# Kernel optimization log

Hardware: AMD Instinct MI355X
Metric: run time of the kernel (lower is better)

The kernel has to match this reference:

```python
import jax, jax.numpy as jnp
import numpy as np

VOCAB = 100000
TAGS = 48
EMB = 256
HID = 512
B, S = 64, 512


def setup_inputs() -> dict:
    key = jax.random.key(0)
    ks = jax.random.split(key, 7)
    sc_e = 1.0 / np.sqrt(EMB)
    sc_h = 1.0 / np.sqrt(HID)
    return {
        "x": jax.random.randint(ks[0], (B, S), 0, VOCAB),
        "emb": jax.random.normal(ks[1], (VOCAB, EMB), jnp.float32),
        "W_ih": jax.random.uniform(ks[2], (4 * HID, EMB), jnp.float32, -sc_e, sc_e),
        "W_hh": jax.random.uniform(ks[3], (4 * HID, HID), jnp.float32, -sc_h, sc_h),
        "b_hh": jax.random.uniform(ks[4], (4 * HID,), jnp.float32, -sc_h, sc_h),
        "fc_W": jax.random.uniform(ks[5], (TAGS, HID), jnp.float32, -sc_h, sc_h),
        "fc_b": jax.random.uniform(ks[6], (TAGS,), jnp.float32, -sc_h, sc_h),
    }


def reference(x, emb, W_ih, W_hh, b_hh, fc_W, fc_b):
    # Embedding lookup: [B,S] -> [B,S,E]
    xe = emb[x]
    # Precompute input projection for all timesteps: [B,S,4H]
    px = jnp.einsum("bse,ge->bsg", xe, W_ih)
    H = W_hh.shape[1]
    Bc = x.shape[0]
    h0 = jnp.zeros((Bc, H), px.dtype)
    c0 = jnp.zeros((Bc, H), px.dtype)

    def step(carry, pxt):
        h, c = carry
        # recurrent dropout prob = 0 -> mask is identity
        gates = pxt + h @ W_hh.T + b_hh  # [B,4H]
        i, f, g, o = jnp.split(gates, 4, axis=-1)
        i = jax.nn.sigmoid(i)
        f = jax.nn.sigmoid(f)
        g = jnp.tanh(g)
        o = jax.nn.sigmoid(o)
        c = f * c + i * g
        h = o * jnp.tanh(c)
        return (h, c), h

    _, hs = jax.lax.scan(step, (h0, c0), jnp.swapaxes(px, 0, 1))
    hs = jnp.swapaxes(hs, 0, 1)  # [B,S,H]
    logits = hs @ fc_W.T + fc_b  # [B,S,TAGS]
    return jax.nn.log_softmax(logits, axis=2)
```

## Files before the change

### kernel.cpp

```cpp
#include <hip/hip_runtime.h>
#include <hip/hip_bf16.h>
#include <hip/hip_fp16.h>

typedef __attribute__((ext_vector_type(8))) short short8;
typedef __attribute__((ext_vector_type(4))) float f32x4;
typedef __attribute__((ext_vector_type(2))) unsigned long long ull2;

#define Hh 512
#define Bb 64
#define Ss 512
#define Gg 2048
#define NROW 32768

static __device__ inline short f2bf(float f) {
    union { float f; unsigned u; } v; v.f = f;
    unsigned r = (v.u + 0x7FFFu + ((v.u >> 16) & 1u)) >> 16;
    return (short)r;
}

static __device__ inline short8 pack_bf8(const float* p) {
    f32x4 u0 = *(const f32x4*)p;
    f32x4 u1 = *(const f32x4*)(p + 4);
    short8 t;
    t[0] = f2bf(u0[0]); t[1] = f2bf(u0[1]); t[2] = f2bf(u0[2]); t[3] = f2bf(u0[3]);
    t[4] = f2bf(u1[0]); t[5] = f2bf(u1[1]); t[6] = f2bf(u1[2]); t[7] = f2bf(u1[3]);
    return t;
}

static __device__ inline float fsigmoid(float x) {
    return __builtin_amdgcn_rcpf(1.f + __builtin_amdgcn_exp2f(x * -1.44269504088896f));
}
static __device__ inline float ftanh(float x) {
    float xc = fminf(fmaxf(x, -15.f), 15.f);
    float e = __builtin_amdgcn_exp2f(xc * 2.88539008177793f);
    return (e - 1.f) / (e + 1.f);
}

__global__ __launch_bounds__(256)
void prep_bf16(const float* __restrict__ wih, const float* __restrict__ fcw,
               short* __restrict__ wih_bf, short* __restrict__ fcw_bf) {
    const int n1 = Gg * 256;
    const int n2 = 48 * Hh;
    for (int i = blockIdx.x * blockDim.x + threadIdx.x; i < n1 + n2;
         i += gridDim.x * blockDim.x) {
        if (i < n1) wih_bf[i] = f2bf(wih[i]);
        else        fcw_bf[i - n1] = f2bf(fcw[i - n1]);
    }
}

__global__ __launch_bounds__(256)
void px_kernel(const int* __restrict__ x, const float* __restrict__ emb,
               const short* __restrict__ wih_bf, const float* __restrict__ bhh,
               _Float16* __restrict__ px) {
    const int w = threadIdx.x >> 6, lane = threadIdx.x & 63;
    const int lr = lane & 15, lc = lane >> 4;
    const int r0 = blockIdx.x * 64 + w * 16;

    short8 a[8];
    const int tok = x[r0 + lr];
    const float* arow = emb + (long)tok * 256;
#pragma unroll
    for (int ks = 0; ks < 8; ks++)
        a[ks] = pack_bf8(arow + ks * 32 + lc * 8);

    for (int g0 = 0; g0 < Gg; g0 += 16) {
        f32x4 acc = {0.f, 0.f, 0.f, 0.f};
#pragma unroll
        for (int ks = 0; ks < 8; ks++) {
            short8 b = *(const short8*)(wih_bf + (g0 + lr) * 256 + ks * 32 + lc * 8);
            acc = __builtin_amdgcn_mfma_f32_16x16x32_bf16(a[ks], b, acc, 0, 0, 0);
        }
        const float bias = bhh[g0 + lr];
#pragma unroll
        for (int i = 0; i < 4; i++) {
            const int r = r0 + lc * 4 + i;
            const int bb = r >> 9, s = r & 511;
            px[((long)s * Bb + bb) * Gg + g0 + lr] = (_Float16)(acc[i] + bias);
        }
    }
}

__global__ __launch_bounds__(512)
void lstm_kernel(const float* __restrict__ whh, const _Float16* __restrict__ px,
                 unsigned int* __restrict__ hbuf32,
                 unsigned int* __restrict__ hs32,
                 int* __restrict__ flags) {
    const int cl  = blockIdx.x & 3;
    const int wgc = blockIdx.x >> 2;
    const int b0 = cl * 16;
    const int J0 = wgc * 64;
    const int w = threadIdx.x >> 6;
    const int lane = threadIdx.x & 63;
    const int lr = lane & 15, lc = lane >> 4;
    const int gt = w & 3;
    const int Jsub = (w >> 2) * 32;

    __shared__ float gates[4][16][64];
    __shared__ __align__(16) unsigned int hlds[16 * 256];

    short8 wf[2][16];
#pragma unroll
    for (int u = 0; u < 2; u++)
#pragma unroll
        for (int ks = 0; ks < 16; ks++)
            wf[u][ks] = pack_bf8(whh + (long)(gt * Hh + J0 + Jsub + u * 16 + lr) * Hh + ks * 32 + lc * 8);

    const int eb = threadIdx.x >> 5;
    const int jp = threadIdx.x & 31;
    float c0 = 0.f, c1 = 0.f;

    const int gr0 = gt * Hh + J0 + Jsub + lr;
    float pf[2][4];
#pragma unroll
    for (int u = 0; u < 2; u++)
#pragma unroll
        for (int i = 0; i < 4; i++)
            pf[u][i] = (float)px[((long)0 * Bb + b0 + lc * 4 + i) * Gg + gr0 + u * 16];

    int* const myflag = flags + cl * 32 + wgc;

#pragma unroll 1
    for (int t = 0; t < Ss; t++) {
        if (threadIdx.x < 8) {
            const int* fp = flags + cl * 32 + threadIdx.x;
            while (__hip_atomic_load(fp, __ATOMIC_RELAXED, __HIP_MEMORY_SCOPE_AGENT) < t)
                __builtin_amdgcn_s_sleep(1);
        }
        __syncthreads();

        {
            const unsigned long long* hb =
                (const unsigned long long*)hbuf32 + (long)(t & 1) * (Bb * Hh / 4);
            int m = threadIdx.x;
#pragma unroll
            for (int k = 0; k < 2; k++, m += 512) {
                const int row = m >> 6;
                const int c   = (m & 63) * 4;
                const unsigned long long* p = hb + (long)(b0 + row) * 128 + (c >> 1);
                unsigned long long q0 = __hip_atomic_load(p,     __ATOMIC_RELAXED, __HIP_MEMORY_SCOPE_AGENT);
                unsigned long long q1 = __hip_atomic_load(p + 1, __ATOMIC_RELAXED, __HIP_MEMORY_SCOPE_AGENT);
                const int sw = c ^ ((row & 7) << 2);
                ull2 q; q[0] = q0; q[1] = q1;
                *(ull2*)&hlds[row * 256 + sw] = q;
            }
        }
        __syncthreads();

        f32x4 acc[2];
#pragma unroll
        for (int u = 0; u < 2; u++) {
            acc[u][0] = pf[u][0]; acc[u][1] = pf[u][1];
            acc[u][2] = pf[u][2]; acc[u][3] = pf[u][3];
        }

#pragma unroll
        for (int ks = 0; ks < 16; ks++) {
            const int c = ks * 16 + lc * 4;
            const short8 af = *(const short8*)&hlds[lr * 256 + (c ^ ((lr & 7) << 2))];
            acc[0] = __builtin_amdgcn_mfma_f32_16x16x32_bf16(af, wf[0][ks], acc[0], 0, 0, 0);
            acc[1] = __builtin_amdgcn_mfma_f32_16x16x32_bf16(af, wf[1][ks], acc[1], 0, 0, 0);
        }

#pragma unroll
        for (int u = 0; u < 2; u++)
#pragma unroll
            for (int i = 0; i < 4; i++)
                gates[gt][lc * 4 + i][Jsub + u * 16 + lr] = acc[u][i];
        __syncthreads();

        unsigned hpack;
        {
            const int j = jp * 2;
            const float gi0 = gates[0][eb][j],   gi1 = gates[0][eb][j + 1];
            const float gf0 = gates[1][eb][j],   gf1 = gates[1][eb][j + 1];
            const float gg0 = gates[2][eb][j],   gg1 = gates[2][eb][j + 1];
            const float go0 = gates[3][eb][j],   go1 = gates[3][eb][j + 1];
            c0 = fsigmoid(gf0) * c0 + fsigmoid(gi0) * ftanh(gg0);
            c1 = fsigmoid(gf1) * c1 + fsigmoid(gi1) * ftanh(gg1);
            const float h0 = fsigmoid(go0) * ftanh(c0);
            const float h1 = fsigmoid(go1) * ftanh(c1);
            hpack = (unsigned)(unsigned short)f2bf(h0)
                  | ((unsigned)(unsigned short)f2bf(h1) << 16);
            unsigned int* hw = hbuf32 + (long)((t + 1) & 1) * (Bb * Hh / 2)
                               + (b0 + eb) * 256 + (J0 >> 1) + jp;
            __hip_atomic_store(hw, hpack, __ATOMIC_RELAXED, __HIP_MEMORY_SCOPE_AGENT);
        }
        __syncthreads();
        if (threadIdx.x == 0)
            __hip_atomic_store(myflag, t + 1, __ATOMIC_RELAXED, __HIP_MEMORY_SCOPE_AGENT);

        const int tn = (t + 1 < Ss) ? t + 1 : t;
#pragma unroll
        for (int u = 0; u < 2; u++)
#pragma unroll
            for (int i = 0; i < 4; i++)
                pf[u][i] = (float)px[((long)tn * Bb + b0 + lc * 4 + i) * Gg + gr0 + u * 16];
        hs32[((long)(b0 + eb) * Ss + t) * 256 + (J0 >> 1) + jp] = hpack;
    }
}

__global__ __launch_bounds__(256)
void fc_kernel(const unsigned short* __restrict__ hs, const short* __restrict__ fcw_bf,
               const float* __restrict__ fcb, float* __restrict__ out) {
    const int w = threadIdx.x >> 6, lane = threadIdx.x & 63;
    const int lr = lane & 15, lc = lane >> 4;
    const int r0 = blockIdx.x * 64 + w * 16;

    short8 af[16];
#pragma unroll
    for (int ks = 0; ks < 16; ks++)
        af[ks] = *(const short8*)((const short*)hs + (long)(r0 + lr) * Hh + ks * 32 + lc * 8);

    f32x4 acc[3];
#pragma unroll
    for (int nt = 0; nt < 3; nt++) {
        f32x4 a_ = {0.f, 0.f, 0.f, 0.f};
#pragma unroll
        for (int ks = 0; ks < 16; ks++) {
            short8 b = *(const short8*)(fcw_bf + (nt * 16 + lr) * Hh + ks * 32 + lc * 8);
            a_ = __builtin_amdgcn_mfma_f32_16x16x32_bf16(af[ks], b, a_, 0, 0, 0);
        }
        acc[nt] = a_;
    }

    const float bb0 = fcb[lr], bb1 = fcb[16 + lr], bb2 = fcb[32 + lr];
#pragma unroll
    for (int i = 0; i < 4; i++) {
        float v0 = acc[0][i] + bb0, v1 = acc[1][i] + bb1, v2 = acc[2][i] + bb2;
        float m = fmaxf(v0, fmaxf(v1, v2));
#pragma unroll
        for (int d = 1; d < 16; d <<= 1) m = fmaxf(m, __shfl_xor(m, d));
        float s = expf(v0 - m) + expf(v1 - m) + expf(v2 - m);
#pragma unroll
        for (int d = 1; d < 16; d <<= 1) s += __shfl_xor(s, d);
        const float lse = m + logf(s);
        const long r = r0 + lc * 4 + i;
        out[r * 48 + lr]      = v0 - lse;
        out[r * 48 + 16 + lr] = v1 - lse;
        out[r * 48 + 32 + lr] = v2 - lse;
    }
}

extern "C" void kernel_launch(void* const* d_in, const int* in_sizes, int n_in,
                              void* d_out, int out_size, void* d_ws, size_t ws_size,
                              hipStream_t stream) {
    const int*   x   = (const int*)d_in[0];
    const float* emb = (const float*)d_in[1];
    const float* wih = (const float*)d_in[2];
    const float* whh = (const float*)d_in[3];
    const float* bhh = (const float*)d_in[4];
    const float* fcw = (const float*)d_in[5];
    const float* fcb = (const float*)d_in[6];
    float* out = (float*)d_out;

    char* ws = (char*)d_ws;
    const size_t off_px    = 0;
    const size_t off_hs    = off_px + (size_t)NROW * Gg * 2;
    const size_t off_hbuf  = off_hs + (size_t)NROW * Hh * 2;
    const size_t off_flags = off_hbuf + 2 * (size_t)Bb * Hh * 2;
    const size_t off_wih   = off_flags + 512;
    const size_t off_fcw   = off_wih + (size_t)Gg * 256 * 2;

    _Float16*     px     = (_Float16*)(ws + off_px);
    unsigned int* hs32   = (unsigned int*)(ws + off_hs);
    unsigned int* hbuf32 = (unsigned int*)(ws + off_hbuf);
    int*          flags  = (int*)(ws + off_flags);
    short*        wih_bf = (short*)(ws + off_wih);
    short*        fcw_bf = (short*)(ws + off_fcw);

    hipMemsetAsync(ws + off_hbuf, 0, 2 * (size_t)Bb * Hh * 2 + 512, stream);
    prep_bf16<<<512, 256, 0, stream>>>(wih, fcw, wih_bf, fcw_bf);
    px_kernel<<<512, 256, 0, stream>>>(x, emb, wih_bf, bhh, px);

    void* args[] = {(void*)&whh, (void*)&px, (void*)&hbuf32, (void*)&hs32, (void*)&flags};
    hipLaunchCooperativeKernel((void*)lstm_kernel, dim3(32), dim3(512), args, 0, stream);

    fc_kernel<<<512, 256, 0, stream>>>((const unsigned short*)hs32, fcw_bf, fcb, out);
}
```

Before: 1.519 ms.

## Replace per-step flag barrier with timestep-tagged hidden-state words

```diff
diff --git a/kernel.cpp b/kernel.cpp
--- a/kernel.cpp
+++ b/kernel.cpp
@@ -4,7 +4,7 @@
 
 typedef __attribute__((ext_vector_type(8))) short short8;
 typedef __attribute__((ext_vector_type(4))) float f32x4;
-typedef __attribute__((ext_vector_type(2))) unsigned long long ull2;
+typedef __attribute__((ext_vector_type(4))) unsigned int u32x4;
 
 #define Hh 512
 #define Bb 64
@@ -82,9 +82,8 @@
 
 __global__ __launch_bounds__(512)
 void lstm_kernel(const float* __restrict__ whh, const _Float16* __restrict__ px,
-                 unsigned int* __restrict__ hbuf32,
-                 unsigned int* __restrict__ hs32,
-                 int* __restrict__ flags) {
+                 unsigned int* __restrict__ hbufT,
+                 unsigned int* __restrict__ hs32) {
     const int cl  = blockIdx.x & 3;
     const int wgc = blockIdx.x >> 2;
     const int b0 = cl * 16;
@@ -95,7 +94,7 @@
     const int gt = w & 3;
     const int Jsub = (w >> 2) * 32;
 
-    __shared__ float gates[4][16][64];
+    __shared__ float gates[4][16][66];
     __shared__ __align__(16) unsigned int hlds[16 * 256];
 
     short8 wf[2][16];
@@ -117,32 +116,42 @@
         for (int i = 0; i < 4; i++)
             pf[u][i] = (float)px[((long)0 * Bb + b0 + lc * 4 + i) * Gg + gr0 + u * 16];
 
-    int* const myflag = flags + cl * 32 + wgc;
+    const int prow = threadIdx.x >> 5;
+    const int pcg  = threadIdx.x & 31;
+    const int csw  = (prow & 7) << 2;
+    const int li0  = prow * 256 + ((pcg * 8) ^ csw);
+    const int li1  = prow * 256 + ((pcg * 8 + 4) ^ csw);
 
 #pragma unroll 1
     for (int t = 0; t < Ss; t++) {
-        if (threadIdx.x < 8) {
-            const int* fp = flags + cl * 32 + threadIdx.x;
-            while (__hip_atomic_load(fp, __ATOMIC_RELAXED, __HIP_MEMORY_SCOPE_AGENT) < t)
-                __builtin_amdgcn_s_sleep(1);
-        }
-        __syncthreads();
-
-        {
-            const unsigned long long* hb =
-                (const unsigned long long*)hbuf32 + (long)(t & 1) * (Bb * Hh / 4);
-            int m = threadIdx.x;
-#pragma unroll
-            for (int k = 0; k < 2; k++, m += 512) {
-                const int row = m >> 6;
-                const int c   = (m & 63) * 4;
-                const unsigned long long* p = hb + (long)(b0 + row) * 128 + (c >> 1);
-                unsigned long long q0 = __hip_atomic_load(p,     __ATOMIC_RELAXED, __HIP_MEMORY_SCOPE_AGENT);
-                unsigned long long q1 = __hip_atomic_load(p + 1, __ATOMIC_RELAXED, __HIP_MEMORY_SCOPE_AGENT);
-                const int sw = c ^ ((row & 7) << 2);
-                ull2 q; q[0] = q0; q[1] = q1;
-                *(ull2*)&hlds[row * 256 + sw] = q;
-            }
+        if (t == 0) {
+            u32x4 z = {0u, 0u, 0u, 0u};
+            *(u32x4*)&hlds[li0] = z;
+            *(u32x4*)&hlds[li1] = z;
+        } else {
+            unsigned long long* pp = (unsigned long long*)
+                (hbufT + (t & 1) * (Bb * Hh) + (b0 + prow) * Hh + pcg * 16);
+            const unsigned long long want2 =
+                ((unsigned long long)(unsigned)t << 48) | ((unsigned long long)(unsigned)t << 16);
+            unsigned long long q[8];
+            unsigned long long bad;
+            do {
+                bad = 0;
+#pragma unroll
+                for (int i = 0; i < 8; i++)
+                    q[i] = __hip_atomic_load(pp + i, __ATOMIC_RELAXED, __HIP_MEMORY_SCOPE_AGENT);
+#pragma unroll
+                for (int i = 0; i < 8; i++)
+                    bad |= (q[i] ^ want2) & 0xFFFF0000FFFF0000ull;
+            } while (bad);
+            unsigned pk[8];
+#pragma unroll
+            for (int i = 0; i < 8; i++)
+                pk[i] = (unsigned)(q[i] & 0xFFFFu) | (((unsigned)(q[i] >> 32) & 0xFFFFu) << 16);
+            u32x4 v0 = {pk[0], pk[1], pk[2], pk[3]};
+            u32x4 v1 = {pk[4], pk[5], pk[6], pk[7]};
+            *(u32x4*)&hlds[li0] = v0;
+            *(u32x4*)&hlds[li1] = v1;
         }
         __syncthreads();
 
@@ -152,7 +161,6 @@
             acc[u][0] = pf[u][0]; acc[u][1] = pf[u][1];
             acc[u][2] = pf[u][2]; acc[u][3] = pf[u][3];
         }
-
 #pragma unroll
         for (int ks = 0; ks < 16; ks++) {
             const int c = ks * 16 + lc * 4;
@@ -168,7 +176,6 @@
                 gates[gt][lc * 4 + i][Jsub + u * 16 + lr] = acc[u][i];
         __syncthreads();
 
-        unsigned hpack;
         {
             const int j = jp * 2;
             const float gi0 = gates[0][eb][j],   gi1 = gates[0][eb][j + 1];
@@ -179,15 +186,17 @@
             c1 = fsigmoid(gf1) * c1 + fsigmoid(gi1) * ftanh(gg1);
             const float h0 = fsigmoid(go0) * ftanh(c0);
             const float h1 = fsigmoid(go1) * ftanh(c1);
-            hpack = (unsigned)(unsigned short)f2bf(h0)
-                  | ((unsigned)(unsigned short)f2bf(h1) << 16);
-            unsigned int* hw = hbuf32 + (long)((t + 1) & 1) * (Bb * Hh / 2)
-                               + (b0 + eb) * 256 + (J0 >> 1) + jp;
-            __hip_atomic_store(hw, hpack, __ATOMIC_RELAXED, __HIP_MEMORY_SCOPE_AGENT);
-        }
-        __syncthreads();
-        if (threadIdx.x == 0)
-            __hip_atomic_store(myflag, t + 1, __ATOMIC_RELAXED, __HIP_MEMORY_SCOPE_AGENT);
+            const unsigned hb0 = (unsigned)(unsigned short)f2bf(h0);
+            const unsigned hb1 = (unsigned)(unsigned short)f2bf(h1);
+            const unsigned tag = (unsigned)(t + 1) << 16;
+            const unsigned long long hv =
+                (unsigned long long)(hb0 | tag) |
+                ((unsigned long long)(hb1 | tag) << 32);
+            unsigned long long* hw = (unsigned long long*)
+                (hbufT + ((t + 1) & 1) * (Bb * Hh) + (b0 + eb) * Hh + J0 + j);
+            __hip_atomic_store(hw, hv, __ATOMIC_RELAXED, __HIP_MEMORY_SCOPE_AGENT);
+            hs32[((long)(b0 + eb) * Ss + t) * 256 + (J0 >> 1) + jp] = hb0 | (hb1 << 16);
+        }
 
         const int tn = (t + 1 < Ss) ? t + 1 : t;
 #pragma unroll
@@ -195,7 +204,6 @@
 #pragma unroll
             for (int i = 0; i < 4; i++)
                 pf[u][i] = (float)px[((long)tn * Bb + b0 + lc * 4 + i) * Gg + gr0 + u * 16];
-        hs32[((long)(b0 + eb) * Ss + t) * 256 + (J0 >> 1) + jp] = hpack;
     }
 }
 
@@ -257,22 +265,20 @@
     const size_t off_px    = 0;
     const size_t off_hs    = off_px + (size_t)NROW * Gg * 2;
     const size_t off_hbuf  = off_hs + (size_t)NROW * Hh * 2;
-    const size_t off_flags = off_hbuf + 2 * (size_t)Bb * Hh * 2;
-    const size_t off_wih   = off_flags + 512;
+    const size_t off_wih   = off_hbuf + 2 * (size_t)Bb * Hh * 4;
     const size_t off_fcw   = off_wih + (size_t)Gg * 256 * 2;
 
     _Float16*     px     = (_Float16*)(ws + off_px);
     unsigned int* hs32   = (unsigned int*)(ws + off_hs);
-    unsigned int* hbuf32 = (unsigned int*)(ws + off_hbuf);
-    int*          flags  = (int*)(ws + off_flags);
+    unsigned int* hbufT  = (unsigned int*)(ws + off_hbuf);
     short*        wih_bf = (short*)(ws + off_wih);
     short*        fcw_bf = (short*)(ws + off_fcw);
 
-    hipMemsetAsync(ws + off_hbuf, 0, 2 * (size_t)Bb * Hh * 2 + 512, stream);
+    hipMemsetAsync(ws + off_hbuf, 0, 2 * (size_t)Bb * Hh * 4, stream);
     prep_bf16<<<512, 256, 0, stream>>>(wih, fcw, wih_bf, fcw_bf);
     px_kernel<<<512, 256, 0, stream>>>(x, emb, wih_bf, bhh, px);
 
-    void* args[] = {(void*)&whh, (void*)&px, (void*)&hbuf32, (void*)&hs32, (void*)&flags};
+    void* args[] = {(void*)&whh, (void*)&px, (void*)&hbufT, (void*)&hs32};
     hipLaunchCooperativeKernel((void*)lstm_kernel, dim3(32), dim3(512), args, 0, stream);
 
     fc_kernel<<<512, 256, 0, stream>>>((const unsigned short*)hs32, fcw_bf, fcb, out);
```

Result: slower. 1.985 ms (+30.7%).

## Use per-wave flags and wave-local polling to drop block barriers in LSTM step

Applied to the files above, without the earlier changes.

```diff
diff --git a/kernel.cpp b/kernel.cpp
--- a/kernel.cpp
+++ b/kernel.cpp
@@ -4,7 +4,7 @@
 
 typedef __attribute__((ext_vector_type(8))) short short8;
 typedef __attribute__((ext_vector_type(4))) float f32x4;
-typedef __attribute__((ext_vector_type(2))) unsigned long long ull2;
+typedef __attribute__((ext_vector_type(4))) unsigned int u32x4;
 
 #define Hh 512
 #define Bb 64
@@ -95,7 +95,7 @@
     const int gt = w & 3;
     const int Jsub = (w >> 2) * 32;
 
-    __shared__ float gates[4][16][64];
+    __shared__ float gates[4][16][66];
     __shared__ __align__(16) unsigned int hlds[16 * 256];
 
     short8 wf[2][16];
@@ -117,32 +117,40 @@
         for (int i = 0; i < 4; i++)
             pf[u][i] = (float)px[((long)0 * Bb + b0 + lc * 4 + i) * Gg + gr0 + u * 16];
 
-    int* const myflag = flags + cl * 32 + wgc;
+    const int srow = lane & 15;
+    const int qi   = lane >> 4;
+    const int scw  = w * 32 + qi * 8;
+    const int ssw  = (srow & 7) << 2;
+    const int sl0  = srow * 256 + (scw ^ ssw);
+    const int sl1  = srow * 256 + ((scw + 4) ^ ssw);
+
+    int* const myflag = flags + (cl * 8 + wgc) * 32 + w;
+    const int* const pollbase = flags + (cl * 8 + w) * 32;
 
 #pragma unroll 1
     for (int t = 0; t < Ss; t++) {
-        if (threadIdx.x < 8) {
-            const int* fp = flags + cl * 32 + threadIdx.x;
-            while (__hip_atomic_load(fp, __ATOMIC_RELAXED, __HIP_MEMORY_SCOPE_AGENT) < t)
-                __builtin_amdgcn_s_sleep(1);
-        }
-        __syncthreads();
-
-        {
-            const unsigned long long* hb =
-                (const unsigned long long*)hbuf32 + (long)(t & 1) * (Bb * Hh / 4);
-            int m = threadIdx.x;
-#pragma unroll
-            for (int k = 0; k < 2; k++, m += 512) {
-                const int row = m >> 6;
-                const int c   = (m & 63) * 4;
-                const unsigned long long* p = hb + (long)(b0 + row) * 128 + (c >> 1);
-                unsigned long long q0 = __hip_atomic_load(p,     __ATOMIC_RELAXED, __HIP_MEMORY_SCOPE_AGENT);
-                unsigned long long q1 = __hip_atomic_load(p + 1, __ATOMIC_RELAXED, __HIP_MEMORY_SCOPE_AGENT);
-                const int sw = c ^ ((row & 7) << 2);
-                ull2 q; q[0] = q0; q[1] = q1;
-                *(ull2*)&hlds[row * 256 + sw] = q;
-            }
+        if (t == 0) {
+            u32x4 z = {0u, 0u, 0u, 0u};
+            *(u32x4*)&hlds[sl0] = z;
+            *(u32x4*)&hlds[sl1] = z;
+        } else {
+            int f;
+            do {
+                f = __hip_atomic_load(pollbase + (lane & 7), __ATOMIC_RELAXED,
+                                      __HIP_MEMORY_SCOPE_AGENT);
+            } while (__any(f < t));
+            asm volatile("" ::: "memory");
+
+            const unsigned long long* hb = (const unsigned long long*)
+                (hbuf32 + (t & 1) * (Bb * Hh / 2) + (b0 + srow) * 256 + scw);
+            unsigned long long q0 = __hip_atomic_load(hb + 0, __ATOMIC_RELAXED, __HIP_MEMORY_SCOPE_AGENT);
+            unsigned long long q1 = __hip_atomic_load(hb + 1, __ATOMIC_RELAXED, __HIP_MEMORY_SCOPE_AGENT);
+            unsigned long long q2 = __hip_atomic_load(hb + 2, __ATOMIC_RELAXED, __HIP_MEMORY_SCOPE_AGENT);
+            unsigned long long q3 = __hip_atomic_load(hb + 3, __ATOMIC_RELAXED, __HIP_MEMORY_SCOPE_AGENT);
+            u32x4 v0 = {(unsigned)q0, (unsigned)(q0 >> 32), (unsigned)q1, (unsigned)(q1 >> 32)};
+            u32x4 v1 = {(unsigned)q2, (unsigned)(q2 >> 32), (unsigned)q3, (unsigned)(q3 >> 32)};
+            *(u32x4*)&hlds[sl0] = v0;
+            *(u32x4*)&hlds[sl1] = v1;
         }
         __syncthreads();
 
@@ -152,7 +160,6 @@
             acc[u][0] = pf[u][0]; acc[u][1] = pf[u][1];
             acc[u][2] = pf[u][2]; acc[u][3] = pf[u][3];
         }
-
 #pragma unroll
         for (int ks = 0; ks < 16; ks++) {
             const int c = ks * 16 + lc * 4;
@@ -181,21 +188,23 @@
             const float h1 = fsigmoid(go1) * ftanh(c1);
             hpack = (unsigned)(unsigned short)f2bf(h0)
                   | ((unsigned)(unsigned short)f2bf(h1) << 16);
-            unsigned int* hw = hbuf32 + (long)((t + 1) & 1) * (Bb * Hh / 2)
+            unsigned int* hw = hbuf32 + ((t + 1) & 1) * (Bb * Hh / 2)
                                + (b0 + eb) * 256 + (J0 >> 1) + jp;
             __hip_atomic_store(hw, hpack, __ATOMIC_RELAXED, __HIP_MEMORY_SCOPE_AGENT);
         }
-        __syncthreads();
-        if (threadIdx.x == 0)
+        asm volatile("s_waitcnt vmcnt(0)" ::: "memory");
+        if (lane == 0)
             __hip_atomic_store(myflag, t + 1, __ATOMIC_RELAXED, __HIP_MEMORY_SCOPE_AGENT);
 
+        hs32[((long)(b0 + eb) * Ss + t) * 256 + (J0 >> 1) + jp] = hpack;
         const int tn = (t + 1 < Ss) ? t + 1 : t;
 #pragma unroll
         for (int u = 0; u < 2; u++)
 #pragma unroll
             for (int i = 0; i < 4; i++)
                 pf[u][i] = (float)px[((long)tn * Bb + b0 + lc * 4 + i) * Gg + gr0 + u * 16];
-        hs32[((long)(b0 + eb) * Ss + t) * 256 + (J0 >> 1) + jp] = hpack;
+        asm volatile("" : "+v"(pf[0][0]), "+v"(pf[0][1]), "+v"(pf[0][2]), "+v"(pf[0][3]),
+                          "+v"(pf[1][0]), "+v"(pf[1][1]), "+v"(pf[1][2]), "+v"(pf[1][3]));
     }
 }
 
@@ -258,7 +267,7 @@
     const size_t off_hs    = off_px + (size_t)NROW * Gg * 2;
     const size_t off_hbuf  = off_hs + (size_t)NROW * Hh * 2;
     const size_t off_flags = off_hbuf + 2 * (size_t)Bb * Hh * 2;
-    const size_t off_wih   = off_flags + 512;
+    const size_t off_wih   = off_flags + 4096;
     const size_t off_fcw   = off_wih + (size_t)Gg * 256 * 2;
 
     _Float16*     px     = (_Float16*)(ws + off_px);
@@ -268,7 +277,7 @@
     short*        wih_bf = (short*)(ws + off_wih);
     short*        fcw_bf = (short*)(ws + off_fcw);
 
-    hipMemsetAsync(ws + off_hbuf, 0, 2 * (size_t)Bb * Hh * 2 + 512, stream);
+    hipMemsetAsync(flags, 0, 4096, stream);
     prep_bf16<<<512, 256, 0, stream>>>(wih, fcw, wih_bf, fcw_bf);
     px_kernel<<<512, 256, 0, stream>>>(x, emb, wih_bf, bhh, px);
 
```

Measured after the change: 1.901 ms. +25.2%, slower.

## Rework LSTM step sync: wave-wide flag polling, skip t=0 h read, unroll by two

Applied to the files above, without the earlier changes.

```diff
diff --git a/kernel.cpp b/kernel.cpp
--- a/kernel.cpp
+++ b/kernel.cpp
@@ -4,7 +4,7 @@
 
 typedef __attribute__((ext_vector_type(8))) short short8;
 typedef __attribute__((ext_vector_type(4))) float f32x4;
-typedef __attribute__((ext_vector_type(2))) unsigned long long ull2;
+typedef __attribute__((ext_vector_type(4))) unsigned int u32x4;
 
 #define Hh 512
 #define Bb 64
@@ -89,13 +89,14 @@
     const int wgc = blockIdx.x >> 2;
     const int b0 = cl * 16;
     const int J0 = wgc * 64;
-    const int w = threadIdx.x >> 6;
-    const int lane = threadIdx.x & 63;
+    const int tid = threadIdx.x;
+    const int w = tid >> 6;
+    const int lane = tid & 63;
     const int lr = lane & 15, lc = lane >> 4;
     const int gt = w & 3;
     const int Jsub = (w >> 2) * 32;
 
-    __shared__ float gates[4][16][64];
+    __shared__ float gates[4][16][66];
     __shared__ __align__(16) unsigned int hlds[16 * 256];
 
     short8 wf[2][16];
@@ -105,98 +106,105 @@
         for (int ks = 0; ks < 16; ks++)
             wf[u][ks] = pack_bf8(whh + (long)(gt * Hh + J0 + Jsub + u * 16 + lr) * Hh + ks * 32 + lc * 8);
 
-    const int eb = threadIdx.x >> 5;
-    const int jp = threadIdx.x & 31;
+    const int eb = tid >> 5;
+    const int jp = tid & 31;
     float c0 = 0.f, c1 = 0.f;
 
     const int gr0 = gt * Hh + J0 + Jsub + lr;
-    float pf[2][4];
+
+    const int srow = tid >> 5;
+    const int scg  = tid & 31;
+    const int q0c  = 2 * scg;
+    const int chi0 = (q0c ^ ((q0c >> 3) & 7) ^ (srow & 7));
+    const int sidx0 = srow * 256 + chi0 * 4;
+    const int sidx1 = srow * 256 + (chi0 ^ 1) * 4;
+
+    int* const myflag = flags + cl * 32 + wgc;
+    const int* const pollbase = flags + cl * 32;
+
+    float pfA[2][4], pfB[2][4];
 #pragma unroll
     for (int u = 0; u < 2; u++)
 #pragma unroll
         for (int i = 0; i < 4; i++)
-            pf[u][i] = (float)px[((long)0 * Bb + b0 + lc * 4 + i) * Gg + gr0 + u * 16];
-
-    int* const myflag = flags + cl * 32 + wgc;
+            pfA[u][i] = (float)px[((long)0 * Bb + b0 + lc * 4 + i) * Gg + gr0 + u * 16];
+
+#define LSTM_STEP(T, PFU, PFN)                                                         \
+    {                                                                                  \
+        const int T_ = (T);                                                            \
+        if (T_ == 0) {                                                                 \
+            u32x4 z = {0u, 0u, 0u, 0u};                                                \
+            *(u32x4*)&hlds[sidx0] = z;                                                 \
+            *(u32x4*)&hlds[sidx1] = z;                                                 \
+        } else {                                                                       \
+            const int* fp = pollbase + (lane & 7);                                     \
+            int fv = __hip_atomic_load(fp, __ATOMIC_RELAXED, __HIP_MEMORY_SCOPE_AGENT);\
+            while (__any(fv < T_))                                                     \
+                fv = __hip_atomic_load(fp, __ATOMIC_RELAXED, __HIP_MEMORY_SCOPE_AGENT);\
+            asm volatile("" ::: "memory");                                             \
+            const unsigned long long* hb = (const unsigned long long*)                 \
+                (hbuf32 + (T_ & 1) * (Bb * Hh / 2) + (b0 + srow) * 256 + scg * 8);     \
+            unsigned long long a0 = __hip_atomic_load(hb + 0, __ATOMIC_RELAXED, __HIP_MEMORY_SCOPE_AGENT); \
+            unsigned long long a1 = __hip_atomic_load(hb + 1, __ATOMIC_RELAXED, __HIP_MEMORY_SCOPE_AGENT); \
+            unsigned long long a2 = __hip_atomic_load(hb + 2, __ATOMIC_RELAXED, __HIP_MEMORY_SCOPE_AGENT); \
+            unsigned long long a3 = __hip_atomic_load(hb + 3, __ATOMIC_RELAXED, __HIP_MEMORY_SCOPE_AGENT); \
+            u32x4 v0 = {(unsigned)a0, (unsigned)(a0 >> 32), (unsigned)a1, (unsigned)(a1 >> 32)}; \
+            u32x4 v1 = {(unsigned)a2, (unsigned)(a2 >> 32), (unsigned)a3, (unsigned)(a3 >> 32)}; \
+            *(u32x4*)&hlds[sidx0] = v0;                                                \
+            *(u32x4*)&hlds[sidx1] = v1;                                                \
+        }                                                                              \
+        __syncthreads();                                         \
+        f32x4 acc0, acc1;                                                              \
+        _Pragma("unroll")                                                              \
+        for (int i = 0; i < 4; i++) { acc0[i] = PFU[0][i]; acc1[i] = PFU[1][i]; }      \
+        _Pragma("unroll")                                                              \
+        for (int ks = 0; ks < 16; ks++) {                                              \
+            const int q = ks * 4 + lc;                                                 \
+            const int chi = q ^ ((q >> 3) & 7) ^ (lr & 7);                             \
+            const short8 af = *(const short8*)&hlds[lr * 256 + chi * 4];               \
+            acc0 = __builtin_amdgcn_mfma_f32_16x16x32_bf16(af, wf[0][ks], acc0, 0, 0, 0); \
+            acc1 = __builtin_amdgcn_mfma_f32_16x16x32_bf16(af, wf[1][ks], acc1, 0, 0, 0); \
+        }                                                                              \
+        _Pragma("unroll")                                                              \
+        for (int i = 0; i < 4; i++) {                                                  \
+            gates[gt][lc * 4 + i][Jsub + lr]      = acc0[i];                           \
+            gates[gt][lc * 4 + i][Jsub + 16 + lr] = acc1[i];                           \
+        }                                                                              \
+        __syncthreads();                                           \
+        unsigned hpack;                                                                \
+        {                                                                              \
+            const float2 gI = *(const float2*)&gates[0][eb][jp * 2];                   \
+            const float2 gF = *(const float2*)&gates[1][eb][jp * 2];                   \
+            const float2 gG = *(const float2*)&gates[2][eb][jp * 2];                   \
+            const float2 gO = *(const float2*)&gates[3][eb][jp * 2];                   \
+            c0 = fsigmoid(gF.x) * c0 + fsigmoid(gI.x) * ftanh(gG.x);                   \
+            c1 = fsigmoid(gF.y) * c1 + fsigmoid(gI.y) * ftanh(gG.y);                   \
+            const float h0 = fsigmoid(gO.x) * ftanh(c0);                               \
+            const float h1 = fsigmoid(gO.y) * ftanh(c1);                               \
+            hpack = (unsigned)(unsigned short)f2bf(h0)                                 \
+                  | ((unsigned)(unsigned short)f2bf(h1) << 16);                        \
+            unsigned int* hw = hbuf32 + ((T_ + 1) & 1) * (Bb * Hh / 2)                 \
+                               + (b0 + eb) * 256 + (J0 >> 1) + jp;                     \
+            __hip_atomic_store(hw, hpack, __ATOMIC_RELAXED, __HIP_MEMORY_SCOPE_AGENT); \
+        }                                                                              \
+        __syncthreads();          \
+        if (tid == 0)                                                                  \
+            __hip_atomic_store(myflag, T_ + 1, __ATOMIC_RELAXED, __HIP_MEMORY_SCOPE_AGENT); \
+        hs32[((long)(b0 + eb) * Ss + T_) * 256 + (J0 >> 1) + jp] = hpack;              \
+        const int tn = (T_ + 1 < Ss) ? T_ + 1 : T_;                                    \
+        _Pragma("unroll")                                                              \
+        for (int u = 0; u < 2; u++)                                                    \
+            _Pragma("unroll")                                                          \
+            for (int i = 0; i < 4; i++)                                                \
+                PFN[u][i] = (float)px[((long)tn * Bb + b0 + lc * 4 + i) * Gg + gr0 + u * 16]; \
+    }
 
 #pragma unroll 1
-    for (int t = 0; t < Ss; t++) {
-        if (threadIdx.x < 8) {
-            const int* fp = flags + cl * 32 + threadIdx.x;
-            while (__hip_atomic_load(fp, __ATOMIC_RELAXED, __HIP_MEMORY_SCOPE_AGENT) < t)
-                __builtin_amdgcn_s_sleep(1);
-        }
-        __syncthreads();
-
-        {
-            const unsigned long long* hb =
-                (const unsigned long long*)hbuf32 + (long)(t & 1) * (Bb * Hh / 4);
-            int m = threadIdx.x;
-#pragma unroll
-            for (int k = 0; k < 2; k++, m += 512) {
-                const int row = m >> 6;
-                const int c   = (m & 63) * 4;
-                const unsigned long long* p = hb + (long)(b0 + row) * 128 + (c >> 1);
-                unsigned long long q0 = __hip_atomic_load(p,     __ATOMIC_RELAXED, __HIP_MEMORY_SCOPE_AGENT);
-                unsigned long long q1 = __hip_atomic_load(p + 1, __ATOMIC_RELAXED, __HIP_MEMORY_SCOPE_AGENT);
-                const int sw = c ^ ((row & 7) << 2);
-                ull2 q; q[0] = q0; q[1] = q1;
-                *(ull2*)&hlds[row * 256 + sw] = q;
-            }
-        }
-        __syncthreads();
-
-        f32x4 acc[2];
-#pragma unroll
-        for (int u = 0; u < 2; u++) {
-            acc[u][0] = pf[u][0]; acc[u][1] = pf[u][1];
-            acc[u][2] = pf[u][2]; acc[u][3] = pf[u][3];
-        }
-
-#pragma unroll
-        for (int ks = 0; ks < 16; ks++) {
-            const int c = ks * 16 + lc * 4;
-            const short8 af = *(const short8*)&hlds[lr * 256 + (c ^ ((lr & 7) << 2))];
-            acc[0] = __builtin_amdgcn_mfma_f32_16x16x32_bf16(af, wf[0][ks], acc[0], 0, 0, 0);
-            acc[1] = __builtin_amdgcn_mfma_f32_16x16x32_bf16(af, wf[1][ks], acc[1], 0, 0, 0);
-        }
-
-#pragma unroll
-        for (int u = 0; u < 2; u++)
-#pragma unroll
-            for (int i = 0; i < 4; i++)
-                gates[gt][lc * 4 + i][Jsub + u * 16 + lr] = acc[u][i];
-        __syncthreads();
-
-        unsigned hpack;
-        {
-            const int j = jp * 2;
-            const float gi0 = gates[0][eb][j],   gi1 = gates[0][eb][j + 1];
-            const float gf0 = gates[1][eb][j],   gf1 = gates[1][eb][j + 1];
-            const float gg0 = gates[2][eb][j],   gg1 = gates[2][eb][j + 1];
-            const float go0 = gates[3][eb][j],   go1 = gates[3][eb][j + 1];
-            c0 = fsigmoid(gf0) * c0 + fsigmoid(gi0) * ftanh(gg0);
-            c1 = fsigmoid(gf1) * c1 + fsigmoid(gi1) * ftanh(gg1);
-            const float h0 = fsigmoid(go0) * ftanh(c0);
-            const float h1 = fsigmoid(go1) * ftanh(c1);
-            hpack = (unsigned)(unsigned short)f2bf(h0)
-                  | ((unsigned)(unsigned short)f2bf(h1) << 16);
-            unsigned int* hw = hbuf32 + (long)((t + 1) & 1) * (Bb * Hh / 2)
-                               + (b0 + eb) * 256 + (J0 >> 1) + jp;
-            __hip_atomic_store(hw, hpack, __ATOMIC_RELAXED, __HIP_MEMORY_SCOPE_AGENT);
-        }
-        __syncthreads();
-        if (threadIdx.x == 0)
-            __hip_atomic_store(myflag, t + 1, __ATOMIC_RELAXED, __HIP_MEMORY_SCOPE_AGENT);
-
-        const int tn = (t + 1 < Ss) ? t + 1 : t;
-#pragma unroll
-        for (int u = 0; u < 2; u++)
-#pragma unroll
-            for (int i = 0; i < 4; i++)
-                pf[u][i] = (float)px[((long)tn * Bb + b0 + lc * 4 + i) * Gg + gr0 + u * 16];
-        hs32[((long)(b0 + eb) * Ss + t) * 256 + (J0 >> 1) + jp] = hpack;
-    }
+    for (int t = 0; t < Ss; t += 2) {
+        LSTM_STEP(t,     pfA, pfB)
+        LSTM_STEP(t + 1, pfB, pfA)
+    }
+#undef LSTM_STEP
 }
 
 __global__ __launch_bounds__(256)
@@ -258,7 +266,7 @@
     const size_t off_hs    = off_px + (size_t)NROW * Gg * 2;
     const size_t off_hbuf  = off_hs + (size_t)NROW * Hh * 2;
     const size_t off_flags = off_hbuf + 2 * (size_t)Bb * Hh * 2;
-    const size_t off_wih   = off_flags + 512;
+    const size_t off_wih   = off_flags + 4096;
     const size_t off_fcw   = off_wih + (size_t)Gg * 256 * 2;
 
     _Float16*     px     = (_Float16*)(ws + off_px);
@@ -268,7 +276,7 @@
     short*        wih_bf = (short*)(ws + off_wih);
     short*        fcw_bf = (short*)(ws + off_fcw);
 
-    hipMemsetAsync(ws + off_hbuf, 0, 2 * (size_t)Bb * Hh * 2 + 512, stream);
+    hipMemsetAsync(flags, 0, 4096, stream);
     prep_bf16<<<512, 256, 0, stream>>>(wih, fcw, wih_bf, fcw_bf);
     px_kernel<<<512, 256, 0, stream>>>(x, emb, wih_bf, bhh, px);
 
```

Result: no change. 1.531 ms (+0.8%).
